# Kernel tuning notes

Hardware: AMD Instinct MI355X
Metric: run time of the kernel (lower is better)

## Reference

```python
import jax, jax.numpy as jnp
import numpy as np

N_HEAD = 16
N_EMBD = 2048


def _rope(x):
    # x: (B, H, L, D). FAITHFUL to source: _apply_rope unpacks (B, L, H, D) on a
    # (B, H, L, D) tensor, so rotation angle = head_index * inv_freq, broadcast over
    # all sequence positions (a latent bug in the original, reproduced exactly).
    B, H, L, D = x.shape
    inv_freq = 1.0 / (10000.0 ** (jnp.arange(0, D, 2, dtype=jnp.float32) / D))  # (D/2,)
    theta = jnp.arange(H, dtype=jnp.float32)[:, None] * inv_freq[None, :]       # (H, D/2)
    cos = jnp.cos(theta)[None, :, None, :]  # (1, H, 1, D/2)
    sin = jnp.sin(theta)[None, :, None, :]
    xp = x.astype(jnp.float32).reshape(B, H, L, D // 2, 2)
    x0, x1 = xp[..., 0], xp[..., 1]
    r0 = x0 * cos - x1 * sin
    r1 = x0 * sin + x1 * cos
    return jnp.stack([r0, r1], axis=-1).reshape(B, H, L, D).astype(x.dtype)


def setup_inputs() -> dict:
    key = jax.random.key(0)
    k1, k2, k3 = jax.random.split(key, 3)
    B, L, C = 2, 2048, N_EMBD
    s = 1.0 / np.sqrt(C).astype(np.float32)
    x = jax.random.normal(k1, (B, L, C), dtype=jnp.float32)
    w_attn = jax.random.normal(k2, (3 * C, C), dtype=jnp.float32) * s
    w_proj = jax.random.normal(k3, (C, C), dtype=jnp.float32) * s
    return {"x": x, "w_attn": w_attn, "w_proj": w_proj}


def reference(x, w_attn, w_proj):
    B, L, C = x.shape
    H = N_HEAD
    D = C // H
    qkv = x @ w_attn.T                       # (B, L, 3C)
    q, k, v = jnp.split(qkv, 3, axis=2)
    q = q.reshape(B, L, H, D).transpose(0, 2, 1, 3)  # (B, H, L, D)
    k = k.reshape(B, L, H, D).transpose(0, 2, 1, 3)
    v = v.reshape(B, L, H, D).transpose(0, 2, 1, 3)
    q = _rope(q)
    k = _rope(k)
    attn = jnp.einsum('bhqd,bhkd->bhqk', q, k) * (1.0 / np.sqrt(D).astype(np.float32))
    causal = jnp.tril(jnp.ones((L, L), dtype=bool))
    attn = jnp.where(causal[None, None], attn, -jnp.inf)
    attn = jax.nn.softmax(attn, axis=-1)
    y = jnp.einsum('bhqk,bhkd->bhqd', attn, v)
    y = y.transpose(0, 2, 1, 3).reshape(B, L, C)
    return y @ w_proj.T
```

## Files before the change

### kernel.cpp

```cpp
#include <hip/hip_runtime.h>

typedef __attribute__((ext_vector_type(8))) short bf16x8;
typedef __attribute__((ext_vector_type(4))) float f32x4;

__device__ __forceinline__ unsigned short f2bf(float f) {
  unsigned int u = __float_as_uint(f);
  u += 0x7FFF + ((u >> 16) & 1);
  return (unsigned short)(u >> 16);
}

__device__ __forceinline__ void gload_lds16(const void* g, void* l) {
  __builtin_amdgcn_global_load_lds(
      (const __attribute__((address_space(1))) unsigned int*)g,
      (__attribute__((address_space(3))) unsigned int*)l,
      16, 0, 0);
}

#define MF(a, b, c) __builtin_amdgcn_mfma_f32_16x16x32_bf16((a), (b), (c), 0, 0, 0)
#define FENCE asm volatile("" ::: "memory")
#define BAR do { FENCE; __builtin_amdgcn_s_barrier(); FENCE; } while (0)

__global__ void cast_all(const float* __restrict__ x,
                         const float* __restrict__ wa,
                         const float* __restrict__ wp,
                         unsigned short* __restrict__ xb,
                         unsigned short* __restrict__ wab,
                         unsigned short* __restrict__ wpb,
                         int n1, int n2, int n4) {
  int stride = gridDim.x * blockDim.x;
  for (int i = blockIdx.x * blockDim.x + threadIdx.x; i < n4; i += stride) {
    const float4* src;
    ushort4* dst;
    int j;
    if (i < n1)      { src = (const float4*)x,  dst = (ushort4*)xb,  j = i; }
    else if (i < n2) { src = (const float4*)wa, dst = (ushort4*)wab, j = i - n1; }
    else             { src = (const float4*)wp, dst = (ushort4*)wpb, j = i - n2; }
    float4 v = src[j];
    ushort4 o;
    o.x = f2bf(v.x); o.y = f2bf(v.y); o.z = f2bf(v.z); o.w = f2bf(v.w);
    dst[j] = o;
  }
}

template<int EPI>
__global__ __launch_bounds__(512, 2)
void gemm8p(const unsigned short* __restrict__ A,
            const unsigned short* __restrict__ Bw,
            float* __restrict__ Cf,
            unsigned short* __restrict__ Qo,
            unsigned short* __restrict__ Ko,
            unsigned short* __restrict__ Vo,
            int M, int N, int K, int Lseq) {
  __shared__ unsigned short Al[2][128 * 64];
  __shared__ unsigned short Bl[2][256 * 64];
  const int tid = threadIdx.x;
  const int lane = tid & 63, w = tid >> 6;
  const int wm = w >> 2, wn = w & 3;
  const int g4 = lane >> 4, r16 = lane & 15;
  const long arow0 = (long)blockIdx.y * 128;
  const long brow0 = (long)blockIdx.x * 256;

#define LDA(db, mf, ks)                                                       \
  (*(const bf16x8*)((const char*)&Al[db][0] +                                 \
                    ((wm * 64 + (mf)*16 + r16) << 7) +                        \
                    ((((ks)*4 + g4) ^ (r16 & 7)) << 4)))
#define LDB(db, nf, ks)                                                       \
  (*(const bf16x8*)((const char*)&Bl[db][0] +                                 \
                    ((wn * 64 + (nf)*16 + r16) << 7) +                        \
                    ((((ks)*4 + g4) ^ (r16 & 7)) << 4)))

#define STGA(db, kt)                                                          \
  do {                                                                        \
    _Pragma("unroll")                                                         \
    for (int c_ = 0; c_ < 2; ++c_) {                                          \
      int off_ = (c_ << 13) + (tid << 4);                                     \
      int row_ = off_ >> 7;                                                   \
      int cbs_ = ((off_ >> 4) & 7) ^ (row_ & 7);                              \
      gload_lds16(A + (arow0 + row_) * (long)K + ((kt) << 6) + cbs_ * 8,      \
                  (char*)&Al[db][0] + off_);                                  \
    }                                                                         \
  } while (0)
#define STGB(db, kt)                                                          \
  do {                                                                        \
    _Pragma("unroll")                                                         \
    for (int c_ = 0; c_ < 4; ++c_) {                                          \
      int off_ = (c_ << 13) + (tid << 4);                                     \
      int row_ = off_ >> 7;                                                   \
      int cbs_ = ((off_ >> 4) & 7) ^ (row_ & 7);                              \
      gload_lds16(Bw + (brow0 + row_) * (long)K + ((kt) << 6) + cbs_ * 8,     \
                  (char*)&Bl[db][0] + off_);                                  \
    }                                                                         \
  } while (0)

  f32x4 acc[4][4];
#pragma unroll
  for (int i = 0; i < 4; ++i)
#pragma unroll
    for (int j = 0; j < 4; ++j) acc[i][j] = (f32x4){0.f, 0.f, 0.f, 0.f};

  bf16x8 b00, b01, b10, b11, b20, b21, b30, b31;
  bf16x8 x0, x1, x2, x3, y0, y1, y2, y3;

#define LOADB(db)                                                             \
  do {                                                                        \
    b00 = LDB(db, 0, 0); b01 = LDB(db, 0, 1);                                 \
    b10 = LDB(db, 1, 0); b11 = LDB(db, 1, 1);                                 \
    b20 = LDB(db, 2, 0); b21 = LDB(db, 2, 1);                                 \
    b30 = LDB(db, 3, 0); b31 = LDB(db, 3, 1);                                 \
  } while (0)

#define PREFA(d0, d1, d2, d3, db, q)                                          \
  do {                                                                        \
    d0 = LDA(db, 2*(q), 0);   d1 = LDA(db, 2*(q), 1);                         \
    d2 = LDA(db, 2*(q)+1, 0); d3 = LDA(db, 2*(q)+1, 1);                       \
  } while (0)

#define MFQ(q, A0, A1, A2, A3)                                                \
  do {                                                                        \
    __builtin_amdgcn_s_setprio(1);                                            \
    acc[2*(q)][0] = MF(A0, b00, acc[2*(q)][0]);                               \
    acc[2*(q)][0] = MF(A1, b01, acc[2*(q)][0]);                               \
    acc[2*(q)][1] = MF(A0, b10, acc[2*(q)][1]);                               \
    acc[2*(q)][1] = MF(A1, b11, acc[2*(q)][1]);                               \
    acc[2*(q)][2] = MF(A0, b20, acc[2*(q)][2]);                               \
    acc[2*(q)][2] = MF(A1, b21, acc[2*(q)][2]);                               \
    acc[2*(q)][3] = MF(A0, b30, acc[2*(q)][3]);                               \
    acc[2*(q)][3] = MF(A1, b31, acc[2*(q)][3]);                               \
    acc[2*(q)+1][0] = MF(A2, b00, acc[2*(q)+1][0]);                           \
    acc[2*(q)+1][0] = MF(A3, b01, acc[2*(q)+1][0]);                           \
    acc[2*(q)+1][1] = MF(A2, b10, acc[2*(q)+1][1]);                           \
    acc[2*(q)+1][1] = MF(A3, b11, acc[2*(q)+1][1]);                           \
    acc[2*(q)+1][2] = MF(A2, b20, acc[2*(q)+1][2]);                           \
    acc[2*(q)+1][2] = MF(A3, b21, acc[2*(q)+1][2]);                           \
    acc[2*(q)+1][3] = MF(A2, b30, acc[2*(q)+1][3]);                           \
    acc[2*(q)+1][3] = MF(A3, b31, acc[2*(q)+1][3]);                           \
    __builtin_amdgcn_s_setprio(0);                                            \
  } while (0)

#define VM4 asm volatile("s_waitcnt vmcnt(4)" ::: "memory")

  const int NT = K >> 6;
  STGB(0, 0); STGA(0, 0); STGB(1, 1);
  VM4;
  BAR;
  LOADB(0);
  PREFA(x0, x1, x2, x3, 0, 0);

  for (int i = 0; i < (NT >> 1); ++i) {
    const int t1 = 2 * i + 1;
    int t2 = 2 * i + 2; if (t2 > NT - 1) t2 = NT - 1;
    int t3 = 2 * i + 3; if (t3 > NT - 1) t3 = NT - 1;
    STGA(1, t1);
    BAR;
    MFQ(0, x0, x1, x2, x3);
    PREFA(y0, y1, y2, y3, 0, 1);
    BAR;
    STGB(0, t2);
    VM4;
    BAR;
    MFQ(1, y0, y1, y2, y3);
    LOADB(1);
    PREFA(x0, x1, x2, x3, 1, 0);
    BAR;
    STGA(0, t2);
    BAR;
    MFQ(0, x0, x1, x2, x3);
    PREFA(y0, y1, y2, y3, 1, 1);
    BAR;
    STGB(1, t3);
    VM4;
    BAR;
    MFQ(1, y0, y1, y2, y3);
    LOADB(0);
    PREFA(x0, x1, x2, x3, 0, 0);
    BAR;
  }
  asm volatile("s_waitcnt vmcnt(0)" ::: "memory");

  const float qscale = 0.08838834764831845f;
#pragma unroll
  for (int mf = 0; mf < 4; ++mf) {
#pragma unroll
    for (int nf = 0; nf < 4; ++nf) {
#pragma unroll
      for (int i = 0; i < 4; ++i) {
        long row = arow0 + wm * 64 + mf * 16 + 4 * g4 + i;
        long col = brow0 + wn * 64 + nf * 16 + r16;
        float v = acc[mf][nf][i];
        if (EPI == 0) {
          Cf[row * N + col] = v;
        } else {
          int which = (int)(col >> 11);
          int h = ((int)col >> 7) & 15;
          int d = (int)col & 127;
          int b = (int)(row >> 11);
          int l = (int)row & 2047;
          long bhead = (long)(b * 16 + h);
          if (which == 0)
            Qo[(bhead * Lseq + l) * 128 + d] = f2bf(v * qscale);
          else if (which == 1)
            Ko[(bhead * Lseq + l) * 128 + d] = f2bf(v);
          else
            Vo[(bhead * 128 + d) * Lseq + l] = f2bf(v);
        }
      }
    }
  }
#undef LDA
#undef LDB
#undef STGA
#undef STGB
#undef LOADB
#undef PREFA
#undef MFQ
#undef VM4
}

__global__ __launch_bounds__(256, 2)
void attn_fwd(const unsigned short* __restrict__ Q,
              const unsigned short* __restrict__ K,
              const unsigned short* __restrict__ Vt,
              unsigned short* __restrict__ Y, int L) {
  const int D = 128;
  const int id = blockIdx.x;
  const int g = id & 7, kk = id >> 3;
  const int bh = (g << 2) + (kk >> 5);
  const int qt = 31 - (kk & 31);
  const int tid = threadIdx.x, lane = tid & 63, w = tid >> 6;
  const int g4 = lane >> 4, r16 = lane & 15;
  const int q0 = qt * 64;

  __shared__ unsigned short Klds[2 * 64 * 128];
  __shared__ unsigned short Vlds[2 * 128 * 64];
  __shared__ unsigned short P[4][16][64];
  __shared__ float corrS[4][16];
  __shared__ float lrunS[4][16];

  const unsigned short* Qh = Q + (long)bh * L * D;
  const unsigned short* Kh = K + (long)bh * L * D;
  const unsigned short* Vh = Vt + (long)bh * D * L;

#define STAGE_TILE(kt_, buf_)                                                 \
  do {                                                                        \
    const int kbase_ = (kt_) * 64;                                            \
    _Pragma("unroll")                                                         \
    for (int r_ = 0; r_ < 4; ++r_) {                                          \
      int off_ = (tid << 4) + (r_ << 12);                                     \
      int krow_ = off_ >> 8, kcb_ = (off_ >> 4) & 15;                         \
      int kcbs_ = kcb_ ^ (krow_ & 7);                                         \
      gload_lds16(Kh + (long)(kbase_ + krow_) * 128 + kcbs_ * 8,              \
                  (char*)Klds + (buf_)*16384 + (w << 10) + (r_ << 12));       \
      int vrow_ = off_ >> 7, vcb_ = (off_ >> 4) & 7;                          \
      int vcbs_ = vcb_ ^ (vrow_ & 7);                                         \
      gload_lds16(Vh + (long)vrow_ * L + kbase_ + vcbs_ * 8,                  \
                  (char*)Vlds + (buf_)*16384 + (w << 10) + (r_ << 12));       \
    }                                                                         \
  } while (0)

  bf16x8 qf[4];
  {
    long qrow = q0 + 16 * w + r16;
#pragma unroll
    for (int ks = 0; ks < 4; ++ks)
      qf[ks] = *(const bf16x8*)(Qh + qrow * D + ks * 32 + g4 * 8);
  }
  f32x4 o[8];
#pragma unroll
  for (int j = 0; j < 8; ++j) o[j] = (f32x4){0.f, 0.f, 0.f, 0.f};
  float mrun = -1e30f, lrun = 0.f;
  const int qg = q0 + 16 * w + r16;
  char* Pl = (char*)&P[w][0][0];

  int cur = 0;
  STAGE_TILE(0, 0);

  for (int kt = 0; kt <= qt; ++kt) {
    if (kt < qt) {
      STAGE_TILE(kt + 1, cur ^ 1);
      asm volatile("s_waitcnt vmcnt(8)" ::: "memory");
    } else {
      asm volatile("s_waitcnt vmcnt(0)" ::: "memory");
    }
    __builtin_amdgcn_s_barrier();

    const char* Kl = (const char*)Klds + cur * 16384;
    const char* Vl = (const char*)Vlds + cur * 16384;

    f32x4 s[4];
#pragma unroll
    for (int nf = 0; nf < 4; ++nf) s[nf] = (f32x4){0.f, 0.f, 0.f, 0.f};
#pragma unroll
    for (int ks = 0; ks < 4; ++ks) {
#pragma unroll
      for (int nf = 0; nf < 4; ++nf) {
        int row = 16 * nf + r16;
        bf16x8 kf = *(const bf16x8*)(Kl + row * 256 +
                                     (((ks * 4 + g4) ^ (row & 7)) << 4));
        s[nf] = MF(kf, qf[ks], s[nf]);
      }
    }

    const bool diag = (kt == qt);
    float rmax = -1e30f;
#pragma unroll
    for (int nf = 0; nf < 4; ++nf)
#pragma unroll
      for (int i = 0; i < 4; ++i) {
        float t = s[nf][i];
        if (diag && (kt * 64 + 16 * nf + 4 * g4 + i) > qg) t = -1e30f;
        s[nf][i] = t;
        rmax = fmaxf(rmax, t);
      }
    rmax = fmaxf(rmax, __shfl_xor(rmax, 16));
    rmax = fmaxf(rmax, __shfl_xor(rmax, 32));

    const bool full = __any(rmax > mrun + 8.0f);
    float corr = 1.f;
    if (full) {
      float mnew = fmaxf(mrun, rmax);
      corr = __expf(mrun - mnew);
      mrun = mnew;
      if (g4 == 0) corrS[w][r16] = corr;
    }

    float rs = 0.f;
#pragma unroll
    for (int nf = 0; nf < 4; ++nf) {
      float p0 = __expf(s[nf][0] - mrun);
      float p1 = __expf(s[nf][1] - mrun);
      float p2 = __expf(s[nf][2] - mrun);
      float p3 = __expf(s[nf][3] - mrun);
      rs += (p0 + p1) + (p2 + p3);
      ushort4 pw;
      pw.x = f2bf(p0); pw.y = f2bf(p1); pw.z = f2bf(p2); pw.w = f2bf(p3);
      *(ushort4*)(Pl + r16 * 128 + (((2 * nf + (g4 >> 1)) ^ (r16 & 7)) << 4) +
                  ((g4 & 1) << 3)) = pw;
    }
    rs += __shfl_xor(rs, 16);
    rs += __shfl_xor(rs, 32);
    lrun = lrun * corr + rs;

    if (full) {
#pragma unroll
      for (int i = 0; i < 4; ++i) {
        float cb = corrS[w][4 * g4 + i];
#pragma unroll
        for (int nf2 = 0; nf2 < 8; ++nf2) o[nf2][i] *= cb;
      }
    }

#pragma unroll
    for (int ks2 = 0; ks2 < 2; ++ks2) {
      bf16x8 pf = *(const bf16x8*)(Pl + r16 * 128 +
                                   (((ks2 * 4 + g4) ^ (r16 & 7)) << 4));
#pragma unroll
      for (int nf2 = 0; nf2 < 8; ++nf2) {
        int row = 16 * nf2 + r16;
        bf16x8 vf = *(const bf16x8*)(Vl + row * 128 +
                                     (((ks2 * 4 + g4) ^ (row & 7)) << 4));
        o[nf2] = MF(pf, vf, o[nf2]);
      }
    }
    FENCE;
    __builtin_amdgcn_s_barrier();
    cur ^= 1;
  }
#undef STAGE_TILE

  if (g4 == 0) lrunS[w][r16] = lrun;
  const int b = bh >> 4, h = bh & 15;
#pragma unroll
  for (int i = 0; i < 4; ++i) {
    float linv = 1.f / lrunS[w][4 * g4 + i];
#pragma unroll
    for (int nf2 = 0; nf2 < 8; ++nf2) {
      long row = (long)b * L + q0 + 16 * w + 4 * g4 + i;
      Y[row * 2048 + h * 128 + 16 * nf2 + r16] = f2bf(o[nf2][i] * linv);
    }
  }
}

extern "C" void kernel_launch(void* const* d_in, const int* in_sizes, int n_in,
                              void* d_out, int out_size, void* d_ws,
                              size_t ws_size, hipStream_t stream) {
  const float* x = (const float*)d_in[0];
  const float* wa = (const float*)d_in[1];
  const float* wp = (const float*)d_in[2];
  float* out = (float*)d_out;
  const int B = 2, L = 2048, C = 2048;
  const int M = B * L;

  unsigned short* xb = (unsigned short*)d_ws;
  unsigned short* wab = xb + (size_t)M * C;
  unsigned short* wpb = wab + (size_t)3 * C * C;
  unsigned short* Qb = wpb + (size_t)C * C;
  unsigned short* Kb = Qb + (size_t)M * C;
  unsigned short* Vb = Kb + (size_t)M * C;
  unsigned short* Yb = Vb + (size_t)M * C;

  const int n1 = M * C / 4;
  const int n2 = n1 + 3 * C * C / 4;
  const int n4 = n2 + C * C / 4;
  cast_all<<<2048, 256, 0, stream>>>(x, wa, wp, xb, wab, wpb, n1, n2, n4);

  gemm8p<1><<<dim3(3 * C / 256, M / 128), 512, 0, stream>>>(
      xb, wab, nullptr, Qb, Kb, Vb, M, 3 * C, C, L);

  attn_fwd<<<1024, 256, 0, stream>>>(Qb, Kb, Vb, Yb, L);

  gemm8p<0><<<dim3(C / 256, M / 128), 512, 0, stream>>>(
      Yb, wpb, out, nullptr, nullptr, nullptr, M, C, C, L);
}
```

Baseline: 287.8 us.

## Process 128 query rows per attention block, two 16-row tiles per wave

Each attention block now covers 128 query rows instead of 64. Each wave holds two 16-row Q fragments, so every K/V tile staged in LDS is reused across twice as many queries, and the grid is halved. The corr and lrun broadcasts now use lane shuffles instead of LDS. In exchange, register pressure rises (two accumulator sets), there are half as many blocks, and waves whose causal limit is earlier sit idle on the last key tile.

New measurement: 293.3 us. No clear change (+1.9%).

```diff
diff --git a/kernel.cpp b/kernel.cpp
--- a/kernel.cpp
+++ b/kernel.cpp
@@ -224,17 +224,18 @@
   const int D = 128;
   const int id = blockIdx.x;
   const int g = id & 7, kk = id >> 3;
-  const int bh = (g << 2) + (kk >> 5);
-  const int qt = 31 - (kk & 31);
+  const int bh = (g << 2) + (kk >> 4);
+  const int qt2 = 15 - (kk & 15);
   const int tid = threadIdx.x, lane = tid & 63, w = tid >> 6;
   const int g4 = lane >> 4, r16 = lane & 15;
-  const int q0 = qt * 64;
-
-  __shared__ unsigned short Klds[2 * 64 * 128];
-  __shared__ unsigned short Vlds[2 * 128 * 64];
-  __shared__ unsigned short P[4][16][64];
-  __shared__ float corrS[4][16];
-  __shared__ float lrunS[4][16];
+  const int q0 = qt2 * 128;
+  const int kthi = 2 * qt2 + 1;
+  const int ktw = 2 * qt2 + (w >> 1);
+
+  __shared__ unsigned short ldsbuf[40960];
+  unsigned short* Klds = ldsbuf;
+  unsigned short* Vlds = ldsbuf + 16384;
+  char* Pw = (char*)(ldsbuf + 32768) + w * 4096;
 
   const unsigned short* Qh = Q + (long)bh * L * D;
   const unsigned short* Kh = K + (long)bh * L * D;
@@ -257,25 +258,31 @@
     }                                                                         \
   } while (0)
 
-  bf16x8 qf[4];
+  bf16x8 qf0[4], qf1[4];
   {
-    long qrow = q0 + 16 * w + r16;
-#pragma unroll
-    for (int ks = 0; ks < 4; ++ks)
-      qf[ks] = *(const bf16x8*)(Qh + qrow * D + ks * 32 + g4 * 8);
-  }
-  f32x4 o[8];
-#pragma unroll
-  for (int j = 0; j < 8; ++j) o[j] = (f32x4){0.f, 0.f, 0.f, 0.f};
-  float mrun = -1e30f, lrun = 0.f;
-  const int qg = q0 + 16 * w + r16;
-  char* Pl = (char*)&P[w][0][0];
+    long qr0 = q0 + 32 * w + r16;
+    long qr1 = qr0 + 16;
+#pragma unroll
+    for (int ks = 0; ks < 4; ++ks) {
+      qf0[ks] = *(const bf16x8*)(Qh + qr0 * D + ks * 32 + g4 * 8);
+      qf1[ks] = *(const bf16x8*)(Qh + qr1 * D + ks * 32 + g4 * 8);
+    }
+  }
+  f32x4 o0[8], o1[8];
+#pragma unroll
+  for (int j = 0; j < 8; ++j) {
+    o0[j] = (f32x4){0.f, 0.f, 0.f, 0.f};
+    o1[j] = (f32x4){0.f, 0.f, 0.f, 0.f};
+  }
+  float mrun0 = -1e30f, mrun1 = -1e30f, lrun0 = 0.f, lrun1 = 0.f;
+  const int qg0 = q0 + 32 * w + r16;
+  const int qg1 = qg0 + 16;
 
   int cur = 0;
   STAGE_TILE(0, 0);
 
-  for (int kt = 0; kt <= qt; ++kt) {
-    if (kt < qt) {
+  for (int kt = 0; kt <= kthi; ++kt) {
+    if (kt < kthi) {
       STAGE_TILE(kt + 1, cur ^ 1);
       asm volatile("s_waitcnt vmcnt(8)" ::: "memory");
     } else {
@@ -283,82 +290,108 @@
     }
     __builtin_amdgcn_s_barrier();
 
-    const char* Kl = (const char*)Klds + cur * 16384;
-    const char* Vl = (const char*)Vlds + cur * 16384;
-
-    f32x4 s[4];
-#pragma unroll
-    for (int nf = 0; nf < 4; ++nf) s[nf] = (f32x4){0.f, 0.f, 0.f, 0.f};
-#pragma unroll
-    for (int ks = 0; ks < 4; ++ks) {
+    if (kt <= ktw) {
+      const char* Kl = (const char*)Klds + cur * 16384;
+      const char* Vl = (const char*)Vlds + cur * 16384;
+
+      f32x4 s0[4], s1[4];
 #pragma unroll
       for (int nf = 0; nf < 4; ++nf) {
-        int row = 16 * nf + r16;
-        bf16x8 kf = *(const bf16x8*)(Kl + row * 256 +
-                                     (((ks * 4 + g4) ^ (row & 7)) << 4));
-        s[nf] = MF(kf, qf[ks], s[nf]);
-      }
-    }
-
-    const bool diag = (kt == qt);
-    float rmax = -1e30f;
-#pragma unroll
-    for (int nf = 0; nf < 4; ++nf)
-#pragma unroll
-      for (int i = 0; i < 4; ++i) {
-        float t = s[nf][i];
-        if (diag && (kt * 64 + 16 * nf + 4 * g4 + i) > qg) t = -1e30f;
-        s[nf][i] = t;
-        rmax = fmaxf(rmax, t);
-      }
-    rmax = fmaxf(rmax, __shfl_xor(rmax, 16));
-    rmax = fmaxf(rmax, __shfl_xor(rmax, 32));
-
-    const bool full = __any(rmax > mrun + 8.0f);
-    float corr = 1.f;
-    if (full) {
-      float mnew = fmaxf(mrun, rmax);
-      corr = __expf(mrun - mnew);
-      mrun = mnew;
-      if (g4 == 0) corrS[w][r16] = corr;
-    }
-
-    float rs = 0.f;
-#pragma unroll
-    for (int nf = 0; nf < 4; ++nf) {
-      float p0 = __expf(s[nf][0] - mrun);
-      float p1 = __expf(s[nf][1] - mrun);
-      float p2 = __expf(s[nf][2] - mrun);
-      float p3 = __expf(s[nf][3] - mrun);
-      rs += (p0 + p1) + (p2 + p3);
-      ushort4 pw;
-      pw.x = f2bf(p0); pw.y = f2bf(p1); pw.z = f2bf(p2); pw.w = f2bf(p3);
-      *(ushort4*)(Pl + r16 * 128 + (((2 * nf + (g4 >> 1)) ^ (r16 & 7)) << 4) +
-                  ((g4 & 1) << 3)) = pw;
-    }
-    rs += __shfl_xor(rs, 16);
-    rs += __shfl_xor(rs, 32);
-    lrun = lrun * corr + rs;
-
-    if (full) {
-#pragma unroll
-      for (int i = 0; i < 4; ++i) {
-        float cb = corrS[w][4 * g4 + i];
-#pragma unroll
-        for (int nf2 = 0; nf2 < 8; ++nf2) o[nf2][i] *= cb;
-      }
-    }
-
-#pragma unroll
-    for (int ks2 = 0; ks2 < 2; ++ks2) {
-      bf16x8 pf = *(const bf16x8*)(Pl + r16 * 128 +
-                                   (((ks2 * 4 + g4) ^ (r16 & 7)) << 4));
-#pragma unroll
-      for (int nf2 = 0; nf2 < 8; ++nf2) {
-        int row = 16 * nf2 + r16;
-        bf16x8 vf = *(const bf16x8*)(Vl + row * 128 +
-                                     (((ks2 * 4 + g4) ^ (row & 7)) << 4));
-        o[nf2] = MF(pf, vf, o[nf2]);
+        s0[nf] = (f32x4){0.f, 0.f, 0.f, 0.f};
+        s1[nf] = (f32x4){0.f, 0.f, 0.f, 0.f};
+      }
+#pragma unroll
+      for (int ks = 0; ks < 4; ++ks) {
+#pragma unroll
+        for (int nf = 0; nf < 4; ++nf) {
+          int row = 16 * nf + r16;
+          bf16x8 kf = *(const bf16x8*)(Kl + row * 256 +
+                                       (((ks * 4 + g4) ^ (row & 7)) << 4));
+          s0[nf] = MF(kf, qf0[ks], s0[nf]);
+          s1[nf] = MF(kf, qf1[ks], s1[nf]);
+        }
+      }
+
+      const bool diag = (kt == ktw);
+      float rmax0 = -1e30f, rmax1 = -1e30f;
+#pragma unroll
+      for (int nf = 0; nf < 4; ++nf)
+#pragma unroll
+        for (int i = 0; i < 4; ++i) {
+          int key = kt * 64 + 16 * nf + 4 * g4 + i;
+          float t0 = s0[nf][i];
+          float t1 = s1[nf][i];
+          if (diag && key > qg0) t0 = -1e30f;
+          if (diag && key > qg1) t1 = -1e30f;
+          s0[nf][i] = t0; s1[nf][i] = t1;
+          rmax0 = fmaxf(rmax0, t0);
+          rmax1 = fmaxf(rmax1, t1);
+        }
+      rmax0 = fmaxf(rmax0, __shfl_xor(rmax0, 16));
+      rmax0 = fmaxf(rmax0, __shfl_xor(rmax0, 32));
+      rmax1 = fmaxf(rmax1, __shfl_xor(rmax1, 16));
+      rmax1 = fmaxf(rmax1, __shfl_xor(rmax1, 32));
+
+      const bool full =
+          __any((rmax0 > mrun0 + 8.0f) || (rmax1 > mrun1 + 8.0f));
+      float corr0 = 1.f, corr1 = 1.f;
+      if (full) {
+        float mn0 = fmaxf(mrun0, rmax0);
+        corr0 = __expf(mrun0 - mn0); mrun0 = mn0;
+        float mn1 = fmaxf(mrun1, rmax1);
+        corr1 = __expf(mrun1 - mn1); mrun1 = mn1;
+      }
+
+      float rs0 = 0.f, rs1 = 0.f;
+#pragma unroll
+      for (int nf = 0; nf < 4; ++nf) {
+        int swz = (((2 * nf + (g4 >> 1)) ^ (r16 & 7)) << 4) + ((g4 & 1) << 3);
+        float a0 = __expf(s0[nf][0] - mrun0), a1 = __expf(s0[nf][1] - mrun0);
+        float a2 = __expf(s0[nf][2] - mrun0), a3 = __expf(s0[nf][3] - mrun0);
+        rs0 += (a0 + a1) + (a2 + a3);
+        ushort4 pw0;
+        pw0.x = f2bf(a0); pw0.y = f2bf(a1); pw0.z = f2bf(a2); pw0.w = f2bf(a3);
+        *(ushort4*)(Pw + r16 * 128 + swz) = pw0;
+        float c0 = __expf(s1[nf][0] - mrun1), c1 = __expf(s1[nf][1] - mrun1);
+        float c2 = __expf(s1[nf][2] - mrun1), c3 = __expf(s1[nf][3] - mrun1);
+        rs1 += (c0 + c1) + (c2 + c3);
+        ushort4 pw1;
+        pw1.x = f2bf(c0); pw1.y = f2bf(c1); pw1.z = f2bf(c2); pw1.w = f2bf(c3);
+        *(ushort4*)(Pw + (16 + r16) * 128 + swz) = pw1;
+      }
+      rs0 += __shfl_xor(rs0, 16);
+      rs0 += __shfl_xor(rs0, 32);
+      rs1 += __shfl_xor(rs1, 16);
+      rs1 += __shfl_xor(rs1, 32);
+      lrun0 = lrun0 * corr0 + rs0;
+      lrun1 = lrun1 * corr1 + rs1;
+
+      if (full) {
+#pragma unroll
+        for (int i = 0; i < 4; ++i) {
+          float cb0 = __shfl(corr0, 4 * g4 + i);
+          float cb1 = __shfl(corr1, 4 * g4 + i);
+#pragma unroll
+          for (int nf2 = 0; nf2 < 8; ++nf2) {
+            o0[nf2][i] *= cb0;
+            o1[nf2][i] *= cb1;
+          }
+        }
+      }
+
+#pragma unroll
+      for (int ks2 = 0; ks2 < 2; ++ks2) {
+        int pswz = ((ks2 * 4 + g4) ^ (r16 & 7)) << 4;
+        bf16x8 pf0 = *(const bf16x8*)(Pw + r16 * 128 + pswz);
+        bf16x8 pf1 = *(const bf16x8*)(Pw + (16 + r16) * 128 + pswz);
+#pragma unroll
+        for (int nf2 = 0; nf2 < 8; ++nf2) {
+          int row = 16 * nf2 + r16;
+          bf16x8 vf = *(const bf16x8*)(Vl + row * 128 +
+                                       (((ks2 * 4 + g4) ^ (row & 7)) << 4));
+          o0[nf2] = MF(pf0, vf, o0[nf2]);
+          o1[nf2] = MF(pf1, vf, o1[nf2]);
+        }
       }
     }
     FENCE;
@@ -367,15 +400,17 @@
   }
 #undef STAGE_TILE
 
-  if (g4 == 0) lrunS[w][r16] = lrun;
   const int b = bh >> 4, h = bh & 15;
 #pragma unroll
   for (int i = 0; i < 4; ++i) {
-    float linv = 1.f / lrunS[w][4 * g4 + i];
+    float linv0 = 1.f / __shfl(lrun0, 4 * g4 + i);
+    float linv1 = 1.f / __shfl(lrun1, 4 * g4 + i);
+    long row0 = (long)b * L + q0 + 32 * w + 4 * g4 + i;
+    long row1 = row0 + 16;
 #pragma unroll
     for (int nf2 = 0; nf2 < 8; ++nf2) {
-      long row = (long)b * L + q0 + 16 * w + 4 * g4 + i;
-      Y[row * 2048 + h * 128 + 16 * nf2 + r16] = f2bf(o[nf2][i] * linv);
+      Y[row0 * 2048 + h * 128 + 16 * nf2 + r16] = f2bf(o0[nf2][i] * linv0);
+      Y[row1 * 2048 + h * 128 + 16 * nf2 + r16] = f2bf(o1[nf2][i] * linv1);
     }
   }
 }
@@ -406,7 +441,7 @@
   gemm8p<1><<<dim3(3 * C / 256, M / 128), 512, 0, stream>>>(
       xb, wab, nullptr, Qb, Kb, Vb, M, 3 * C, C, L);
 
-  attn_fwd<<<1024, 256, 0, stream>>>(Qb, Kb, Vb, Yb, L);
+  attn_fwd<<<512, 256, 0, stream>>>(Qb, Kb, Vb, Yb, L);
 
   gemm8p<0><<<dim3(C / 256, M / 128), 512, 0, stream>>>(
       Yb, wpb, out, nullptr, nullptr, nullptr, M, C, C, L);
```
